# Kernel tuning notes

Measured on AMD Instinct MI355X. Metric: run time of the kernel, lower is better.

## Reference

```python
import jax, jax.numpy as jnp
import numpy as np
from jax import lax

WINDOW = 8
MAX_VAL = 1.0
C1 = (0.01 * MAX_VAL) ** 2
C2 = (0.03 * MAX_VAL) ** 2


def _box_sum(x):
    # Equivalent to conv2d with an all-ones WINDOW x WINDOW kernel, groups=C, VALID padding.
    return lax.reduce_window(x, 0.0, lax.add,
                             window_dimensions=(1, 1, WINDOW, WINDOW),
                             window_strides=(1, 1, 1, 1),
                             padding='VALID')


def setup_inputs() -> dict:
    key = jax.random.key(0)
    k1, k2 = jax.random.split(key)
    shape = (32, 3, 512, 512)  # NCHW, C=3 per groups=3 conv
    groundtruth = jax.random.uniform(k1, shape, dtype=jnp.float32)
    noisy_img = jax.random.uniform(k2, shape, dtype=jnp.float32)
    return {"groundtruth": groundtruth, "noisy_img": noisy_img}


def reference(groundtruth, noisy_img):
    mu1 = _box_sum(groundtruth)
    mu2 = _box_sum(noisy_img)
    mu1_sq = mu1 * mu1
    mu2_sq = mu2 * mu2
    mu1_mu2 = mu1 * mu2
    sigma1_sq = _box_sum(groundtruth * groundtruth) - mu1_sq
    sigma2_sq = _box_sum(noisy_img * noisy_img) - mu2_sq
    sigma12 = _box_sum(groundtruth * noisy_img) - mu1_mu2
    ssim_map = ((2.0 * mu1_mu2 + C1) * (2.0 * sigma12 + C2)) / (
        (mu1_sq + mu2_sq + C1) * (sigma1_sq + sigma2_sq + C2))
    return jnp.mean(1.0 - ssim_map)
```

## Files before the change

kernel.cpp:

```cpp
#include <hip/hip_runtime.h>


#define W 512
#define H 512
#define OW 505
#define OH 505
#define TH 32
#define NSTRIP ((OH + TH - 1) / TH)
#define NIMG 96
#define NPIX (96.0 * 505.0 * 505.0)

__device__ __forceinline__ float4 ld4(const float* p) { return *(const float4*)p; }
__device__ __forceinline__ float4 f4add(float4 a, float4 b) {
    return make_float4(a.x + b.x, a.y + b.y, a.z + b.z, a.w + b.w);
}
__device__ __forceinline__ float4 f4sub(float4 a, float4 b) {
    return make_float4(a.x - b.x, a.y - b.y, a.z - b.z, a.w - b.w);
}
__device__ __forceinline__ float4 f4mul(float4 a, float4 b) {
    return make_float4(a.x * b.x, a.y * b.y, a.z * b.z, a.w * b.w);
}

__global__ void zero_ws(double* p) { *p = 0.0; }

__global__ void finalize(const double* p, float* out) {
    out[0] = 1.0f - (float)(*p / NPIX);
}

__global__ void __launch_bounds__(128, 2)
ssim_main(const float* __restrict__ gt, const float* __restrict__ ni,
          double* __restrict__ acc_out)
{
    const int t   = threadIdx.x;
    const int c0  = t * 4;
    const int img = blockIdx.y;
    const int R0  = blockIdx.x * TH;
    const int R1  = min(R0 + TH, OH);

    const float C1 = 1e-4f;
    const float C2 = 9e-4f;

    const float* gx = gt + (size_t)img * (W * H) + c0;
    const float* gy = ni + (size_t)img * (W * H) + c0;

    __shared__ float vbuf[2][5][520];
    __shared__ float wpart[2];

    float4 ring_x[8], ring_y[8];
    float4 vsx  = make_float4(0, 0, 0, 0);
    float4 vsy  = make_float4(0, 0, 0, 0);
    float4 vsxx = make_float4(0, 0, 0, 0);
    float4 vsyy = make_float4(0, 0, 0, 0);
    float4 vsxy = make_float4(0, 0, 0, 0);

#pragma unroll
    for (int k = 0; k < 7; ++k) {
        float4 x = ld4(gx + (size_t)(R0 + k) * W);
        float4 y = ld4(gy + (size_t)(R0 + k) * W);
        ring_x[k] = x; ring_y[k] = y;
        vsx  = f4add(vsx, x);
        vsy  = f4add(vsy, y);
        vsxx = f4add(vsxx, f4mul(x, x));
        vsyy = f4add(vsyy, f4mul(y, y));
        vsxy = f4add(vsxy, f4mul(x, y));
    }
    ring_x[7] = make_float4(0, 0, 0, 0);
    ring_y[7] = make_float4(0, 0, 0, 0);

    float4 px = ld4(gx + (size_t)(R0 + 7) * W);
    float4 py = ld4(gy + (size_t)(R0 + 7) * W);

    float acc = 0.0f;

#define HORIZ(q, v) {                                                     \
        float4 n1 = *(float4*)&vbuf[b][q][c0 + 4];                        \
        float4 n2 = *(float4*)&vbuf[b][q][c0 + 8];                        \
        float s = v.x + v.y + v.z + v.w + n1.x + n1.y + n1.z + n1.w;      \
        B[q][0] = s;                                                      \
        s += n2.x - v.x; B[q][1] = s;                                     \
        s += n2.y - v.y; B[q][2] = s;                                     \
        s += n2.z - v.z; B[q][3] = s;                                     \
    }

#define ROWBODY(k, slot) {                                                \
        const int r = rbase + (k);                                        \
        if (r < R1) {                                  \
            float4 cx = px, cy = py;                                      \
            if (r + 1 < R1) {    \
                px = ld4(gx + (size_t)(r + 8) * W);                       \
                py = ld4(gy + (size_t)(r + 8) * W);                       \
            }                                                             \
            float4 ox = ring_x[slot], oy = ring_y[slot];                  \
            vsx  = f4add(f4sub(vsx,  ox),           cx);                  \
            vsy  = f4add(f4sub(vsy,  oy),           cy);                  \
            vsxx = f4add(f4sub(vsxx, f4mul(ox, ox)), f4mul(cx, cx));      \
            vsyy = f4add(f4sub(vsyy, f4mul(oy, oy)), f4mul(cy, cy));      \
            vsxy = f4add(f4sub(vsxy, f4mul(ox, oy)), f4mul(cx, cy));      \
            ring_x[slot] = cx; ring_y[slot] = cy;                         \
            const int b = r & 1;                                          \
            *(float4*)&vbuf[b][0][c0] = vsx;                              \
            *(float4*)&vbuf[b][1][c0] = vsy;                              \
            *(float4*)&vbuf[b][2][c0] = vsxx;                             \
            *(float4*)&vbuf[b][3][c0] = vsyy;                             \
            *(float4*)&vbuf[b][4][c0] = vsxy;                             \
            __syncthreads();                                              \
            float B[5][4];                                                \
            HORIZ(0, vsx); HORIZ(1, vsy); HORIZ(2, vsxx);                 \
            HORIZ(3, vsyy); HORIZ(4, vsxy);                               \
            _Pragma("unroll")                                             \
            for (int j = 0; j < 4; ++j) {                                 \
                float Sx = B[0][j], Sy = B[1][j];                         \
                float Sxx = B[2][j], Syy = B[3][j], Sxy = B[4][j];        \
                float mu12 = Sx * Sy;                                     \
                float n1v = 2.0f * mu12 + C1;                             \
                float n2v = 2.0f * (Sxy - mu12) + C2;                     \
                float d1  = Sx * Sx + Sy * Sy + C1;                       \
                float d2  = (Sxx - Sx * Sx) + (Syy - Sy * Sy) + C2;       \
                float sv  = (n1v * n2v) / (d1 * d2);                      \
                if (c0 + j < OW) acc += sv;                               \
            }                                                             \
        }                                                                 \
    }

    for (int rbase = R0; rbase < R1; rbase += 8) {
        ROWBODY(0, 7)
        ROWBODY(1, 0)
        ROWBODY(2, 1)
        ROWBODY(3, 2)
        ROWBODY(4, 3)
        ROWBODY(5, 4)
        ROWBODY(6, 5)
        ROWBODY(7, 6)
    }

#pragma unroll
    for (int off = 32; off > 0; off >>= 1) acc += __shfl_down(acc, off);
    const int wave = t >> 6, lane = t & 63;
    if (lane == 0) wpart[wave] = acc;
    __syncthreads();
    if (t == 0) atomicAdd(acc_out, (double)(wpart[0] + wpart[1]));
}

extern "C" void kernel_launch(void* const* d_in, const int* in_sizes, int n_in,
                              void* d_out, int out_size, void* d_ws, size_t ws_size,
                              hipStream_t stream) {
    const float* gt = (const float*)d_in[0];
    const float* ni = (const float*)d_in[1];
    double* acc = (double*)d_ws;

    zero_ws<<<1, 1, 0, stream>>>(acc);
    dim3 grid(NSTRIP, NIMG);
    ssim_main<<<grid, 128, 0, stream>>>(gt, ni, acc);
    finalize<<<1, 1, 0, stream>>>(acc, (float*)d_out);
}
```

Before: 233.1 us.

## Merge squared sums, halve strip height, use rcp and single LDS buffer

Merges the sum-of-x² and sum-of-y² sliding accumulators into one, because only their sum enters the SSIM denominator. This cuts one horizontal pass and one LDS plane. The double-buffered LDS becomes a single buffer with a second barrier per row. The strip height drops from 32 to 16 rows and launch bounds now request 4 blocks per SM, aiming for more parallelism. The exact division is replaced by a hardware reciprocal approximation. The extra barrier and the larger halo-reload overhead from shorter strips offset part of the savings.

```diff
diff --git a/kernel.cpp b/kernel.cpp
--- a/kernel.cpp
+++ b/kernel.cpp
@@ -5,7 +5,7 @@
 #define H 512
 #define OW 505
 #define OH 505
-#define TH 32
+#define TH 16
 #define NSTRIP ((OH + TH - 1) / TH)
 #define NIMG 96
 #define NPIX (96.0 * 505.0 * 505.0)
@@ -27,7 +27,7 @@
     out[0] = 1.0f - (float)(*p / NPIX);
 }
 
-__global__ void __launch_bounds__(128, 2)
+__global__ void __launch_bounds__(128, 4)
 ssim_main(const float* __restrict__ gt, const float* __restrict__ ni,
           double* __restrict__ acc_out)
 {
@@ -43,26 +43,24 @@
     const float* gx = gt + (size_t)img * (W * H) + c0;
     const float* gy = ni + (size_t)img * (W * H) + c0;
 
-    __shared__ float vbuf[2][5][520];
+    __shared__ float vbuf[4][520];
     __shared__ float wpart[2];
 
     float4 ring_x[8], ring_y[8];
-    float4 vsx  = make_float4(0, 0, 0, 0);
-    float4 vsy  = make_float4(0, 0, 0, 0);
-    float4 vsxx = make_float4(0, 0, 0, 0);
-    float4 vsyy = make_float4(0, 0, 0, 0);
-    float4 vsxy = make_float4(0, 0, 0, 0);
+    float4 vsx = make_float4(0, 0, 0, 0);
+    float4 vsy = make_float4(0, 0, 0, 0);
+    float4 vsq = make_float4(0, 0, 0, 0);
+    float4 vsp = make_float4(0, 0, 0, 0);
 
 #pragma unroll
     for (int k = 0; k < 7; ++k) {
         float4 x = ld4(gx + (size_t)(R0 + k) * W);
         float4 y = ld4(gy + (size_t)(R0 + k) * W);
         ring_x[k] = x; ring_y[k] = y;
-        vsx  = f4add(vsx, x);
-        vsy  = f4add(vsy, y);
-        vsxx = f4add(vsxx, f4mul(x, x));
-        vsyy = f4add(vsyy, f4mul(y, y));
-        vsxy = f4add(vsxy, f4mul(x, y));
+        vsx = f4add(vsx, x);
+        vsy = f4add(vsy, y);
+        vsq = f4add(vsq, f4add(f4mul(x, x), f4mul(y, y)));
+        vsp = f4add(vsp, f4mul(x, y));
     }
     ring_x[7] = make_float4(0, 0, 0, 0);
     ring_y[7] = make_float4(0, 0, 0, 0);
@@ -73,9 +71,10 @@
     float acc = 0.0f;
 
 #define HORIZ(q, v) {                                                     \
-        float4 n1 = *(float4*)&vbuf[b][q][c0 + 4];                        \
-        float4 n2 = *(float4*)&vbuf[b][q][c0 + 8];                        \
-        float s = v.x + v.y + v.z + v.w + n1.x + n1.y + n1.z + n1.w;      \
+        float4 n1 = *(float4*)&vbuf[q][c0 + 4];                           \
+        float4 n2 = *(float4*)&vbuf[q][c0 + 8];                           \
+        float s = ((v.x + v.y) + (v.z + v.w)) +                           \
+                  ((n1.x + n1.y) + (n1.z + n1.w));                        \
         B[q][0] = s;                                                      \
         s += n2.x - v.x; B[q][1] = s;                                     \
         s += n2.y - v.y; B[q][2] = s;                                     \
@@ -91,32 +90,31 @@
                 py = ld4(gy + (size_t)(r + 8) * W);                       \
             }                                                             \
             float4 ox = ring_x[slot], oy = ring_y[slot];                  \
-            vsx  = f4add(f4sub(vsx,  ox),           cx);                  \
-            vsy  = f4add(f4sub(vsy,  oy),           cy);                  \
-            vsxx = f4add(f4sub(vsxx, f4mul(ox, ox)), f4mul(cx, cx));      \
-            vsyy = f4add(f4sub(vsyy, f4mul(oy, oy)), f4mul(cy, cy));      \
-            vsxy = f4add(f4sub(vsxy, f4mul(ox, oy)), f4mul(cx, cy));      \
+            vsx = f4add(f4sub(vsx, ox), cx);                              \
+            vsy = f4add(f4sub(vsy, oy), cy);                              \
+            vsq = f4add(vsq, f4sub(f4add(f4mul(cx, cx), f4mul(cy, cy)),   \
+                                   f4add(f4mul(ox, ox), f4mul(oy, oy)))); \
+            vsp = f4add(vsp, f4sub(f4mul(cx, cy), f4mul(ox, oy)));        \
             ring_x[slot] = cx; ring_y[slot] = cy;                         \
-            const int b = r & 1;                                          \
-            *(float4*)&vbuf[b][0][c0] = vsx;                              \
-            *(float4*)&vbuf[b][1][c0] = vsy;                              \
-            *(float4*)&vbuf[b][2][c0] = vsxx;                             \
-            *(float4*)&vbuf[b][3][c0] = vsyy;                             \
-            *(float4*)&vbuf[b][4][c0] = vsxy;                             \
+            *(float4*)&vbuf[0][c0] = vsx;                                 \
+            *(float4*)&vbuf[1][c0] = vsy;                                 \
+            *(float4*)&vbuf[2][c0] = vsq;                                 \
+            *(float4*)&vbuf[3][c0] = vsp;                                 \
             __syncthreads();                                              \
-            float B[5][4];                                                \
-            HORIZ(0, vsx); HORIZ(1, vsy); HORIZ(2, vsxx);                 \
-            HORIZ(3, vsyy); HORIZ(4, vsxy);                               \
+            float B[4][4];                                                \
+            HORIZ(0, vsx); HORIZ(1, vsy); HORIZ(2, vsq); HORIZ(3, vsp);   \
+            __syncthreads();  \
             _Pragma("unroll")                                             \
             for (int j = 0; j < 4; ++j) {                                 \
                 float Sx = B[0][j], Sy = B[1][j];                         \
-                float Sxx = B[2][j], Syy = B[3][j], Sxy = B[4][j];        \
+                float Sq = B[2][j], Sp = B[3][j];                         \
                 float mu12 = Sx * Sy;                                     \
                 float n1v = 2.0f * mu12 + C1;                             \
-                float n2v = 2.0f * (Sxy - mu12) + C2;                     \
-                float d1  = Sx * Sx + Sy * Sy + C1;                       \
-                float d2  = (Sxx - Sx * Sx) + (Syy - Sy * Sy) + C2;       \
-                float sv  = (n1v * n2v) / (d1 * d2);                      \
+                float n2v = 2.0f * (Sp - mu12) + C2;                      \
+                float sx2 = Sx * Sx, sy2 = Sy * Sy;                       \
+                float d1  = sx2 + sy2 + C1;                               \
+                float d2  = (Sq - sx2 - sy2) + C2;                        \
+                float sv  = (n1v * n2v) * __builtin_amdgcn_rcpf(d1 * d2); \
                 if (c0 + j < OW) acc += sv;                               \
             }                                                             \
         }                                                                 \
```

Result: slower. 251.1 us (+7.7%).
